# Kernel tuning notes

Measured on AMD Instinct MI355X. Metric: run time of the kernel, lower is better.

The kernel has to match this reference:

```python
import jax, jax.numpy as jnp
import numpy as np

T, N, E, IN_DIM, OUT_DIM, K = 4, 50000, 800000, 128, 128, 3


def setup_inputs() -> dict:
    key = jax.random.key(0)
    ks = jax.random.split(key, 6)
    x = jax.random.normal(ks[0], (T, N, IN_DIM), dtype=jnp.float32)
    edge_row = jax.random.randint(ks[1], (E,), 0, N, dtype=jnp.int64)
    edge_col = jax.random.randint(ks[2], (E,), 0, N, dtype=jnp.int64)
    edge_val = jax.random.uniform(ks[3], (E,), dtype=jnp.float32)
    # xavier_uniform per [in,out] slice: bound = sqrt(6/(in+out))
    bound = float(np.sqrt(6.0 / (IN_DIM + OUT_DIM)))
    weight = jax.random.uniform(ks[4], (T, K, IN_DIM, OUT_DIM), dtype=jnp.float32,
                                minval=-bound, maxval=bound)
    bias = jnp.zeros((T, OUT_DIM), dtype=jnp.float32)
    return {"x": x, "edge_row": edge_row, "edge_col": edge_col,
            "edge_val": edge_val, "weight": weight, "bias": bias}


def _spmm_batched(edge_row, edge_col, edge_val, h):
    # h: [T, N, C]; sparse A (COO) applied to flattened [N, T*C] features
    t, n, c = h.shape
    h_flat = jnp.transpose(h, (1, 0, 2)).reshape(n, t * c)      # [N, T*C]
    msg = edge_val[:, None] * h_flat[edge_col]                  # [E, T*C]
    out = jax.ops.segment_sum(msg, edge_row, num_segments=n)    # [N, T*C]
    return jnp.transpose(out.reshape(n, t, c), (1, 0, 2))       # [T, N, C]


def reference(x, edge_row, edge_col, edge_val, weight, bias):
    # Chebyshev recurrence: T_0 = x, T_1 = L x, T_k = 2 L T_{k-1} - T_{k-2}
    tx_0 = x
    out = jnp.einsum('tni,tio->tno', tx_0, weight[:, 0])
    tx_1 = _spmm_batched(edge_row, edge_col, edge_val, x)
    out = out + jnp.einsum('tni,tio->tno', tx_1, weight[:, 1])
    for k in range(2, K):
        tx_2 = 2.0 * _spmm_batched(edge_row, edge_col, edge_val, tx_1) - tx_0
        out = out + jnp.einsum('tni,tio->tno', tx_2, weight[:, k])
        tx_0, tx_1 = tx_1, tx_2
    return out + bias[:, None, :]
```

## Files before the change

kernel.cpp:

```cpp
#include <hip/hip_runtime.h>
#include <hip/hip_bf16.h>

#define T_ 4
#define N_ 50000
#define E_ 800000
#define C_ 128
#define K_ 3
#define TC_ 512
#define UNROLL_ 16
#define GROWS_ 256

typedef __hip_bfloat16 bf16;
typedef __attribute__((ext_vector_type(4))) float f32x4;
typedef __attribute__((ext_vector_type(8))) short bf16x8;
typedef __attribute__((ext_vector_type(4))) short s16x4;

__device__ inline short bf16bits(float f) {
    bf16 h = __float2bfloat16(f);
    union { bf16 h; short s; } u; u.h = h; return u.s;
}
__device__ inline float bf16f(short s) {
    union { bf16 h; short s; } u; u.s = s; return __bfloat162float(u.h);
}


__global__ void count_kernel(const int* __restrict__ row, int* __restrict__ counts) {
    int e = blockIdx.x * blockDim.x + threadIdx.x;
    if (e < E_) atomicAdd(&counts[row[e]], 1);
}

__global__ __launch_bounds__(1024) void scan_kernel(const int* __restrict__ counts,
                                                    int* __restrict__ starts,
                                                    int* __restrict__ cursors) {
    __shared__ int wsum[16];
    __shared__ int carry_s;
    int tid = threadIdx.x;
    int wave = tid >> 6, lane = tid & 63;
    if (tid == 0) carry_s = 0;
    __syncthreads();
    for (int base = 0; base < N_; base += 1024) {
        int i = base + tid;
        int v = (i < N_) ? counts[i] : 0;
        int s = v;
        #pragma unroll
        for (int off = 1; off < 64; off <<= 1) {
            int u = __shfl_up(s, off, 64);
            if (lane >= off) s += u;
        }
        if (lane == 63) wsum[wave] = s;
        __syncthreads();
        if (wave == 0) {
            int w = (lane < 16) ? wsum[lane] : 0;
            #pragma unroll
            for (int off = 1; off < 16; off <<= 1) {
                int u = __shfl_up(w, off, 64);
                if (lane >= off) w += u;
            }
            if (lane < 16) wsum[lane] = w;
        }
        __syncthreads();
        int carry = carry_s;
        int wbase = (wave == 0) ? 0 : wsum[wave - 1];
        int incl = carry + wbase + s;
        if (i < N_) {
            starts[i]  = incl - v;
            cursors[i] = incl - v;
        }
        __syncthreads();
        if (tid == 1023) carry_s = incl;
        __syncthreads();
    }
    if (tid == 0) starts[N_] = carry_s;
}

__global__ void scatter_kernel(const int* __restrict__ row, const int* __restrict__ col,
                               const float* __restrict__ val, int* __restrict__ cursors,
                               int* __restrict__ scol, float* __restrict__ sval) {
    int e = blockIdx.x * blockDim.x + threadIdx.x;
    if (e < E_) {
        int p = atomicAdd(&cursors[row[e]], 1);
        scol[p] = col[e];
        sval[p] = val[e];
    }
}


__global__ __launch_bounds__(256) void convert_kernel(const float* __restrict__ x,
                                                      bf16* __restrict__ xb) {
    int t   = blockIdx.y;
    int idx = blockIdx.x * 256 + threadIdx.x;
    int n = idx >> 5, q = idx & 31;
    f32x4 v = *(const f32x4*)(x + ((size_t)t * N_ + n) * C_ + q * 4);
    s16x4 o;
    #pragma unroll
    for (int j = 0; j < 4; ++j) o[j] = bf16bits(v[j]);
    *(s16x4*)(xb + (size_t)n * TC_ + t * C_ + q * 4) = o;
}


__global__ __launch_bounds__(256) void prep_w_kernel(const float* __restrict__ weight,
                                                     bf16* __restrict__ Wt) {
    __shared__ float lds[32][33];
    int b = blockIdx.x;
    int ts = b >> 4, tile = b & 15;
    int t = ts / 3, kk = ts % 3;
    int it = (tile >> 2) * 32, ot = (tile & 3) * 32;
    int tx = threadIdx.x & 31, ty = threadIdx.x >> 5;
    const float* W  = weight + ((size_t)t * K_ + kk) * C_ * C_;
    const float* W2 = weight + ((size_t)t * K_ + 2) * C_ * C_;
    #pragma unroll
    for (int r = 0; r < 4; ++r) {
        int i = it + ty + r * 8, o = ot + tx;
        float w = W[(size_t)i * C_ + o];
        if (kk == 0)      w -= W2[(size_t)i * C_ + o];
        else if (kk == 2) w *= 2.f;
        lds[ty + r * 8][tx] = w;
    }
    __syncthreads();
    #pragma unroll
    for (int r = 0; r < 4; ++r) {
        int o = ot + ty + r * 8, i = it + tx;
        Wt[((size_t)ts * C_ + o) * C_ + i] = __float2bfloat16(lds[tx][ty + r * 8]);
    }
}


__global__ __launch_bounds__(128) void spmm_kernel(const int* __restrict__ starts,
                                                   const int* __restrict__ scol,
                                                   const float* __restrict__ sval,
                                                   const bf16* __restrict__ src,
                                                   bf16* __restrict__ dst) {
    int n   = blockIdx.x;
    int ch  = threadIdx.x * 4;
    int s  = starts[n];
    int e1 = starts[n + 1];
    const bf16* sb = src + ch;
    f32x4 acc = {0.f, 0.f, 0.f, 0.f};
    for (int e = s; e < e1; e += UNROLL_) {
        int   cc[UNROLL_];
        float vv[UNROLL_];
        #pragma unroll
        for (int j = 0; j < UNROLL_; ++j) {
            int ee = e + j;
            bool ok = ee < e1;
            cc[j] = ok ? scol[ee] : 0;
            vv[j] = ok ? sval[ee] : 0.f;
        }
        s16x4 g[UNROLL_];
        #pragma unroll
        for (int j = 0; j < UNROLL_; ++j)
            g[j] = *(const s16x4*)(sb + (size_t)cc[j] * TC_);
        #pragma unroll
        for (int j = 0; j < UNROLL_; ++j) {
            #pragma unroll
            for (int q = 0; q < 4; ++q)
                acc[q] += vv[j] * bf16f(g[j][q]);
        }
    }
    s16x4 o;
    #pragma unroll
    for (int j = 0; j < 4; ++j) o[j] = bf16bits(acc[j]);
    *(s16x4*)(dst + (size_t)n * TC_ + ch) = o;
}


__global__ __launch_bounds__(512) void gemm_kernel(const float* __restrict__ x,
                                                   const bf16* __restrict__ tx1b,
                                                   const bf16* __restrict__ ub,
                                                   const bf16* __restrict__ Wt,
                                                   const float* __restrict__ bias,
                                                   float* __restrict__ out) {
    __shared__ __align__(16) short Bs[128][136];
    int t  = blockIdx.y;
    int m0 = blockIdx.x * GROWS_;
    int tid  = threadIdx.x;
    int wave = tid >> 6, lane = tid & 63;
    int l15 = lane & 15, l4 = lane >> 4;
    int krow = l4 * 8;

    int sr = tid >> 4;
    int ss = (tid & 15) * 8;

    f32x4 acc[2][8];
    #pragma unroll
    for (int i = 0; i < 2; ++i)
        #pragma unroll
        for (int j = 0; j < 8; ++j) acc[i][j] = (f32x4){0.f, 0.f, 0.f, 0.f};

    size_t tslice = (size_t)t * N_ * C_;
    int row[2];
    #pragma unroll
    for (int mf = 0; mf < 2; ++mf) {
        int gr = m0 + wave * 32 + mf * 16 + l15;
        row[mf] = gr < N_ ? gr : N_ - 1;
    }
    const bf16* wt = Wt + (size_t)t * 3 * C_ * C_;

    int4 pf[4];
    #pragma unroll
    for (int i = 0; i < 4; ++i)
        pf[i] = *(const int4*)(wt + (size_t)(i * 32 + sr) * C_ + ss);
    #pragma unroll
    for (int i = 0; i < 4; ++i)
        *(int4*)&Bs[i * 32 + sr][ss] = pf[i];
    __syncthreads();

    #pragma unroll
    for (int sid = 0; sid < 3; ++sid) {
        if (sid < 2) {
            const bf16* wn = wt + (size_t)(sid + 1) * C_ * C_;
            #pragma unroll
            for (int i = 0; i < 4; ++i)
                pf[i] = *(const int4*)(wn + (size_t)(i * 32 + sr) * C_ + ss);
        }
        #pragma unroll
        for (int kk = 0; kk < 4; ++kk) {
            int i0 = kk * 32;
            bf16x8 bfr[8];
            #pragma unroll
            for (int nf = 0; nf < 8; ++nf)
                bfr[nf] = *(bf16x8*)&Bs[nf * 16 + l15][i0 + krow];
            bf16x8 a[2];
            if (sid == 0) {
                #pragma unroll
                for (int mf = 0; mf < 2; ++mf) {
                    const float* p = x + tslice + (size_t)row[mf] * C_ + i0 + krow;
                    f32x4 u0 = *(const f32x4*)p;
                    f32x4 u1 = *(const f32x4*)(p + 4);
                    bf16x8 av;
                    #pragma unroll
                    for (int j = 0; j < 4; ++j) { av[j] = bf16bits(u0[j]); av[j + 4] = bf16bits(u1[j]); }
                    a[mf] = av;
                }
            } else {
                const bf16* src = (sid == 1) ? tx1b : ub;
                #pragma unroll
                for (int mf = 0; mf < 2; ++mf)
                    a[mf] = *(const bf16x8*)(src + (size_t)row[mf] * TC_ + t * C_ + i0 + krow);
            }
            #pragma unroll
            for (int mf = 0; mf < 2; ++mf)
                #pragma unroll
                for (int nf = 0; nf < 8; ++nf)
                    acc[mf][nf] = __builtin_amdgcn_mfma_f32_16x16x32_bf16(a[mf], bfr[nf], acc[mf][nf], 0, 0, 0);
        }
        __syncthreads();
        if (sid < 2) {
            #pragma unroll
            for (int i = 0; i < 4; ++i)
                *(int4*)&Bs[i * 32 + sr][ss] = pf[i];
            __syncthreads();
        }
    }

    const float* bs = bias + (size_t)t * C_;
    float* ot = out + tslice;
    #pragma unroll
    for (int nf = 0; nf < 8; ++nf) {
        int gc = nf * 16 + l15;
        float bv = bs[gc];
        #pragma unroll
        for (int mf = 0; mf < 2; ++mf) {
            #pragma unroll
            for (int reg = 0; reg < 4; ++reg) {
                int gr = m0 + wave * 32 + mf * 16 + l4 * 4 + reg;
                if (gr < N_) ot[(size_t)gr * C_ + gc] = acc[mf][nf][reg] + bv;
            }
        }
    }
}


extern "C" void kernel_launch(void* const* d_in, const int* in_sizes, int n_in,
                              void* d_out, int out_size, void* d_ws, size_t ws_size,
                              hipStream_t stream) {
    const float* x      = (const float*)d_in[0];
    const int*   erow   = (const int*)d_in[1];
    const int*   ecol   = (const int*)d_in[2];
    const float* eval   = (const float*)d_in[3];
    const float* weight = (const float*)d_in[4];
    const float* bias   = (const float*)d_in[5];
    float* out = (float*)d_out;

    char* ws = (char*)d_ws;
    size_t off = 0;
    auto alloc = [&](size_t bytes) -> void* {
        void* p = ws + off;
        off += (bytes + 255) & ~(size_t)255;
        return p;
    };
    int*   counts  = (int*)alloc((N_ + 1) * sizeof(int));
    int*   starts  = (int*)alloc((N_ + 1) * sizeof(int));
    int*   cursors = (int*)alloc((size_t)N_ * sizeof(int));
    int*   scol    = (int*)alloc((size_t)E_ * sizeof(int));
    float* sval    = (float*)alloc((size_t)E_ * sizeof(float));
    bf16*  bufA    = (bf16*)alloc((size_t)N_ * TC_ * sizeof(bf16));
    bf16*  bufB    = (bf16*)alloc((size_t)N_ * TC_ * sizeof(bf16));
    bf16*  Wt      = (bf16*)alloc((size_t)T_ * K_ * C_ * C_ * sizeof(bf16));

    hipMemsetAsync(counts, 0, (N_ + 1) * sizeof(int), stream);
    count_kernel<<<(E_ + 255) / 256, 256, 0, stream>>>(erow, counts);
    scan_kernel<<<1, 1024, 0, stream>>>(counts, starts, cursors);
    scatter_kernel<<<(E_ + 255) / 256, 256, 0, stream>>>(erow, ecol, eval, cursors, scol, sval);
    prep_w_kernel<<<T_ * K_ * 16, 256, 0, stream>>>(weight, Wt);
    dim3 cg(N_ * 32 / 256, T_);
    convert_kernel<<<cg, 256, 0, stream>>>(x, bufA);
    spmm_kernel<<<N_, 128, 0, stream>>>(starts, scol, sval, bufA, bufB);
    spmm_kernel<<<N_, 128, 0, stream>>>(starts, scol, sval, bufB, bufA);
    dim3 g((N_ + GROWS_ - 1) / GROWS_, T_);
    gemm_kernel<<<g, 512, 0, stream>>>(x, bufB, bufA, Wt, bias, out);
}
```

Baseline: 658.0 us.

## Pack CSR col/val pairs, vectorize count/scatter, reuse bf16 x in GEMM

```diff
diff --git a/kernel.cpp b/kernel.cpp
--- a/kernel.cpp
+++ b/kernel.cpp
@@ -25,8 +25,16 @@
 
 
 __global__ void count_kernel(const int* __restrict__ row, int* __restrict__ counts) {
-    int e = blockIdx.x * blockDim.x + threadIdx.x;
-    if (e < E_) atomicAdd(&counts[row[e]], 1);
+    int i = (blockIdx.x * blockDim.x + threadIdx.x) * 4;
+    if (i + 3 < E_) {
+        int4 r = *(const int4*)(row + i);
+        atomicAdd(&counts[r.x], 1);
+        atomicAdd(&counts[r.y], 1);
+        atomicAdd(&counts[r.z], 1);
+        atomicAdd(&counts[r.w], 1);
+    } else {
+        for (int j = i; j < E_; ++j) atomicAdd(&counts[row[j]], 1);
+    }
 }
 
 __global__ __launch_bounds__(1024) void scan_kernel(const int* __restrict__ counts,
@@ -75,12 +83,16 @@
 
 __global__ void scatter_kernel(const int* __restrict__ row, const int* __restrict__ col,
                                const float* __restrict__ val, int* __restrict__ cursors,
-                               int* __restrict__ scol, float* __restrict__ sval) {
-    int e = blockIdx.x * blockDim.x + threadIdx.x;
-    if (e < E_) {
-        int p = atomicAdd(&cursors[row[e]], 1);
-        scol[p] = col[e];
-        sval[p] = val[e];
+                               int2* __restrict__ packed) {
+    int i = (blockIdx.x * blockDim.x + threadIdx.x) * 2;
+    if (i < E_) {
+        int2   r = *(const int2*)(row + i);
+        int2   c = *(const int2*)(col + i);
+        float2 v = *(const float2*)(val + i);
+        int p0 = atomicAdd(&cursors[r.x], 1);
+        packed[p0] = make_int2(c.x, __float_as_int(v.x));
+        int p1 = atomicAdd(&cursors[r.y], 1);
+        packed[p1] = make_int2(c.y, __float_as_int(v.y));
     }
 }
 
@@ -126,8 +138,7 @@
 
 
 __global__ __launch_bounds__(128) void spmm_kernel(const int* __restrict__ starts,
-                                                   const int* __restrict__ scol,
-                                                   const float* __restrict__ sval,
+                                                   const int2* __restrict__ packed,
                                                    const bf16* __restrict__ src,
                                                    bf16* __restrict__ dst) {
     int n   = blockIdx.x;
@@ -137,24 +148,22 @@
     const bf16* sb = src + ch;
     f32x4 acc = {0.f, 0.f, 0.f, 0.f};
     for (int e = s; e < e1; e += UNROLL_) {
-        int   cc[UNROLL_];
-        float vv[UNROLL_];
+        int2 ev[UNROLL_];
         #pragma unroll
         for (int j = 0; j < UNROLL_; ++j) {
             int ee = e + j;
-            bool ok = ee < e1;
-            cc[j] = ok ? scol[ee] : 0;
-            vv[j] = ok ? sval[ee] : 0.f;
+            ev[j] = (ee < e1) ? packed[ee] : make_int2(0, 0);
         }
         s16x4 g[UNROLL_];
         #pragma unroll
         for (int j = 0; j < UNROLL_; ++j)
-            g[j] = *(const s16x4*)(sb + (size_t)cc[j] * TC_);
+            g[j] = *(const s16x4*)(sb + (size_t)ev[j].x * TC_);
         #pragma unroll
         for (int j = 0; j < UNROLL_; ++j) {
+            float v = __int_as_float(ev[j].y);
             #pragma unroll
             for (int q = 0; q < 4; ++q)
-                acc[q] += vv[j] * bf16f(g[j][q]);
+                acc[q] += v * bf16f(g[j][q]);
         }
     }
     s16x4 o;
@@ -164,7 +173,9 @@
 }
 
 
+template <int XBF16>
 __global__ __launch_bounds__(512) void gemm_kernel(const float* __restrict__ x,
+                                                   const bf16* __restrict__ xb,
                                                    const bf16* __restrict__ tx1b,
                                                    const bf16* __restrict__ ub,
                                                    const bf16* __restrict__ Wt,
@@ -221,7 +232,13 @@
             for (int nf = 0; nf < 8; ++nf)
                 bfr[nf] = *(bf16x8*)&Bs[nf * 16 + l15][i0 + krow];
             bf16x8 a[2];
-            if (sid == 0) {
+            if (XBF16 || sid > 0) {
+                const bf16* src = XBF16 ? (sid == 0 ? xb : (sid == 1 ? tx1b : ub))
+                                        : (sid == 1 ? tx1b : ub);
+                #pragma unroll
+                for (int mf = 0; mf < 2; ++mf)
+                    a[mf] = *(const bf16x8*)(src + (size_t)row[mf] * TC_ + t * C_ + i0 + krow);
+            } else {
                 #pragma unroll
                 for (int mf = 0; mf < 2; ++mf) {
                     const float* p = x + tslice + (size_t)row[mf] * C_ + i0 + krow;
@@ -232,11 +249,6 @@
                     for (int j = 0; j < 4; ++j) { av[j] = bf16bits(u0[j]); av[j + 4] = bf16bits(u1[j]); }
                     a[mf] = av;
                 }
-            } else {
-                const bf16* src = (sid == 1) ? tx1b : ub;
-                #pragma unroll
-                for (int mf = 0; mf < 2; ++mf)
-                    a[mf] = *(const bf16x8*)(src + (size_t)row[mf] * TC_ + t * C_ + i0 + krow);
             }
             #pragma unroll
             for (int mf = 0; mf < 2; ++mf)
@@ -289,24 +301,29 @@
         off += (bytes + 255) & ~(size_t)255;
         return p;
     };
-    int*   counts  = (int*)alloc((N_ + 1) * sizeof(int));
-    int*   starts  = (int*)alloc((N_ + 1) * sizeof(int));
-    int*   cursors = (int*)alloc((size_t)N_ * sizeof(int));
-    int*   scol    = (int*)alloc((size_t)E_ * sizeof(int));
-    float* sval    = (float*)alloc((size_t)E_ * sizeof(float));
-    bf16*  bufA    = (bf16*)alloc((size_t)N_ * TC_ * sizeof(bf16));
-    bf16*  bufB    = (bf16*)alloc((size_t)N_ * TC_ * sizeof(bf16));
-    bf16*  Wt      = (bf16*)alloc((size_t)T_ * K_ * C_ * C_ * sizeof(bf16));
+    const size_t bufsz = (size_t)N_ * TC_ * sizeof(bf16);
+    int*  counts  = (int*)alloc((N_ + 1) * sizeof(int));
+    int*  starts  = (int*)alloc((N_ + 1) * sizeof(int));
+    int*  cursors = (int*)alloc((size_t)N_ * sizeof(int));
+    int2* packed  = (int2*)alloc((size_t)E_ * sizeof(int2));
+    bf16* Wt      = (bf16*)alloc((size_t)T_ * K_ * C_ * C_ * sizeof(bf16));
+    bf16* bufX    = (bf16*)alloc(bufsz);
+    bf16* bufT    = (bf16*)alloc(bufsz);
+    bool three = (ws_size >= off + bufsz + 256);
+    bf16* bufU = three ? (bf16*)alloc(bufsz) : bufX;
 
     hipMemsetAsync(counts, 0, (N_ + 1) * sizeof(int), stream);
-    count_kernel<<<(E_ + 255) / 256, 256, 0, stream>>>(erow, counts);
+    count_kernel<<<(E_ / 4 + 255) / 256, 256, 0, stream>>>(erow, counts);
     scan_kernel<<<1, 1024, 0, stream>>>(counts, starts, cursors);
-    scatter_kernel<<<(E_ + 255) / 256, 256, 0, stream>>>(erow, ecol, eval, cursors, scol, sval);
+    scatter_kernel<<<(E_ / 2 + 255) / 256, 256, 0, stream>>>(erow, ecol, eval, cursors, packed);
     prep_w_kernel<<<T_ * K_ * 16, 256, 0, stream>>>(weight, Wt);
     dim3 cg(N_ * 32 / 256, T_);
-    convert_kernel<<<cg, 256, 0, stream>>>(x, bufA);
-    spmm_kernel<<<N_, 128, 0, stream>>>(starts, scol, sval, bufA, bufB);
-    spmm_kernel<<<N_, 128, 0, stream>>>(starts, scol, sval, bufB, bufA);
+    convert_kernel<<<cg, 256, 0, stream>>>(x, bufX);
+    spmm_kernel<<<N_, 128, 0, stream>>>(starts, packed, bufX, bufT);
+    spmm_kernel<<<N_, 128, 0, stream>>>(starts, packed, bufT, bufU);
     dim3 g((N_ + GROWS_ - 1) / GROWS_, T_);
-    gemm_kernel<<<g, 512, 0, stream>>>(x, bufB, bufA, Wt, bias, out);
-}
+    if (three)
+        gemm_kernel<1><<<g, 512, 0, stream>>>(x, bufX, bufT, bufU, Wt, bias, out);
+    else
+        gemm_kernel<0><<<g, 512, 0, stream>>>(x, bufX, bufT, bufU, Wt, bias, out);
+}
```

Result: faster. 627.6 us (-4.6%).
